# Optimization experiments

Hardware: AMD Instinct MI355X
Metric: run time of the kernel (lower is better)

Reference implementation:

```python
import jax, jax.numpy as jnp
import numpy as np
from jax import lax

B, C, H, W = 8, 256, 32, 32
HEADS = 8
NUM_OFF = 9
OFF_SCALE = 0.1


def setup_inputs() -> dict:
    key = jax.random.key(0)
    ks = jax.random.split(key, 8)
    f = lambda k, s, sc: jax.random.normal(k, s, dtype=jnp.float32) * sc
    return {
        'query_map': f(ks[0], (B, C, H, W), 1.0),
        'kv_map': f(ks[1], (B, C, H, W), 1.0),
        'Wq': f(ks[2], (C, C), C ** -0.5),
        'Wk': f(ks[3], (C, C), C ** -0.5),
        'Wv': f(ks[4], (C, C), C ** -0.5),
        'Woff1': f(ks[5], (C // 2, C, 3, 3), (C * 9) ** -0.5),
        'boff1': jnp.zeros((C // 2,), jnp.float32),
        'Woff2': f(ks[6], (NUM_OFF * 2, C // 2), (C // 2) ** -0.5),
        'boff2': jnp.zeros((NUM_OFF * 2,), jnp.float32),
        'Wout': f(ks[7], (C, C), C ** -0.5),
        'bout': jnp.zeros((C,), jnp.float32),
    }


def grid_sample_bilinear_border(img, grid):
    """img: (B,C,H,W); grid: (B,H,W,2) with (x,y) in [-1,1], align_corners=True,
    padding_mode='border'. Returns (B,C,H,W)."""
    Bn, Cn, Hn, Wn = img.shape
    x = (grid[..., 0] + 1.0) * 0.5 * (Wn - 1)
    y = (grid[..., 1] + 1.0) * 0.5 * (Hn - 1)
    # border padding: clamp continuous coords into the valid range
    x = jnp.clip(x, 0.0, Wn - 1)
    y = jnp.clip(y, 0.0, Hn - 1)
    x0 = jnp.floor(x)
    y0 = jnp.floor(y)
    wx = x - x0
    wy = y - y0
    x0i = x0.astype(jnp.int32)
    y0i = y0.astype(jnp.int32)
    x1i = jnp.minimum(x0i + 1, Wn - 1)
    y1i = jnp.minimum(y0i + 1, Hn - 1)
    flat = img.reshape(Bn, Cn, Hn * Wn)

    def gat(iy, ix):
        idx = (iy * Wn + ix).reshape(Bn, 1, -1)  # broadcasts over channels
        return jnp.take_along_axis(flat, idx, axis=2)

    v00 = gat(y0i, x0i)
    v01 = gat(y0i, x1i)
    v10 = gat(y1i, x0i)
    v11 = gat(y1i, x1i)
    wxf = wx.reshape(Bn, 1, -1)
    wyf = wy.reshape(Bn, 1, -1)
    out = (v00 * (1 - wxf) + v01 * wxf) * (1 - wyf) + (v10 * (1 - wxf) + v11 * wxf) * wyf
    return out.reshape(Bn, Cn, Hn, Wn)


def reference(query_map, kv_map, Wq, Wk, Wv, Woff1, boff1, Woff2, boff2, Wout, bout):
    Bn, Cn, Hn, Wn = query_map.shape
    hd = Cn // HEADS
    # 1x1 conv projections as channel einsums
    q = jnp.einsum('oc,bchw->bohw', Wq, query_map)
    # offset network: 3x3 conv -> relu -> 1x1 conv
    h1 = lax.conv_general_dilated(q, Woff1, (1, 1), 'SAME',
                                  dimension_numbers=('NCHW', 'OIHW', 'NCHW'))
    h1 = jax.nn.relu(h1 + boff1[None, :, None, None])
    offsets = jnp.einsum('oc,bchw->bohw', Woff2, h1) + boff2[None, :, None, None]
    offsets = offsets.reshape(Bn, NUM_OFF, 2, Hn, Wn)
    offset = offsets[:, 0] * OFF_SCALE  # (B,2,H,W); ch0 -> x, ch1 -> y
    # normalized base grid in [-1,1] (align_corners=True convention)
    gx = jnp.linspace(-1.0, 1.0, Wn, dtype=q.dtype)[None, :]  # (1,W)
    gy = jnp.linspace(-1.0, 1.0, Hn, dtype=q.dtype)[:, None]  # (H,1)
    vx = gx[None] + offset[:, 0]  # (B,H,W)
    vy = gy[None] + offset[:, 1]
    vgrid = jnp.stack([vx, vy], axis=-1)  # (B,H,W,2)
    kv_sampled = grid_sample_bilinear_border(kv_map, vgrid)
    k = jnp.einsum('oc,bchw->bohw', Wk, kv_sampled)
    v = jnp.einsum('oc,bchw->bohw', Wv, kv_sampled)
    # (B,C,H,W) -> (B,heads,HW,hd)
    def to_heads(t):
        return t.reshape(Bn, HEADS, hd, Hn * Wn).transpose(0, 1, 3, 2)
    qh, kh, vh = to_heads(q), to_heads(k), to_heads(v)
    scale = hd ** -0.5
    attn = jnp.einsum('bhqd,bhkd->bhqk', qh, kh) * scale
    attn = jax.nn.softmax(attn, axis=-1)
    out = jnp.einsum('bhqk,bhkd->bhqd', attn, vh)
    out = out.transpose(0, 1, 3, 2).reshape(Bn, Cn, Hn, Wn)
    out = jnp.einsum('oc,bchw->bohw', Wout, out) + bout[None, :, None, None]
    return out
```

## Files before the change

### kernel.cpp

```cpp
#include <hip/hip_runtime.h>

#define HW_ 1024

typedef __attribute__((ext_vector_type(8))) short bf16x8;
typedef __attribute__((ext_vector_type(4))) short bf16x4;
typedef __attribute__((ext_vector_type(4))) float f32x4;

__device__ inline unsigned short f2bf(float f) {
  unsigned int u = __float_as_uint(f);
  u += 0x7FFF + ((u >> 16) & 1);
  return (unsigned short)(u >> 16);
}
__device__ inline unsigned short f2bf_fast(float f) {
  return (unsigned short)((__float_as_uint(f) + 0x8000u) >> 16);
}
__device__ inline float bf2f(unsigned short h) {
  return __uint_as_float(((unsigned int)h) << 16);
}
__device__ inline void async_copy16(const void* g, void* l) {
  __builtin_amdgcn_global_load_lds(
      (const __attribute__((address_space(1))) unsigned int*)g,
      (__attribute__((address_space(3))) unsigned int*)l, 16, 0, 0);
}

__global__ __launch_bounds__(256) void fused0(
    const float* __restrict__ kv,
    const float* __restrict__ Wq, const float* __restrict__ Wk,
    const float* __restrict__ Wv, const float* __restrict__ Wo,
    const float* __restrict__ Woff1, const float* __restrict__ Xf,
    short* __restrict__ WH, short* __restrict__ WL, short* __restrict__ wb,
    float* __restrict__ kvT,
    short* __restrict__ Yt, short* __restrict__ Yh2, short* __restrict__ Yl2)
{
  __shared__ float T[256][33];
  __shared__ short Bsh[32][40];
  __shared__ short Bsl[32][40];
  const int bid = blockIdx.x, t = threadIdx.x;

  if (bid < 512) {
    const int w    = t >> 6;
    const int lane = t & 63;
    const int ln   = lane & 15;
    const int qd   = lane >> 4;
    const int bp0  = (bid & 255) * 32;
    const int om   = (bid >> 8) * 128 + w * 32;
    const int bB   = bp0 >> 10, p0l = bp0 & 1023;

    f32x4 acc[2][2] = {};
#pragma unroll
    for (int k0 = 0; k0 < 256; k0 += 32) {
      __syncthreads();
      {
        int pp = t & 31, cg = t >> 5;
        float fv[4];
#pragma unroll
        for (int j = 0; j < 4; ++j)
          fv[j] = Xf[((size_t)(bB * 256 + k0 + cg * 4 + j)) * HW_ + p0l + pp];
        bf16x4 h4, l4;
#pragma unroll
        for (int j = 0; j < 4; ++j) {
          unsigned short h = f2bf(fv[j]);
          h4[j] = (short)h;
          l4[j] = (short)f2bf(fv[j] - bf2f(h));
        }
        *(bf16x4*)&Bsh[pp][cg * 4] = h4;
        *(bf16x4*)&Bsl[pp][cg * 4] = l4;
      }
      __syncthreads();

      bf16x8 Ah[2], Al[2], Bh[2], Bl[2];
#pragma unroll
      for (int mt = 0; mt < 2; ++mt) {
        const float* ws = &Wq[((size_t)(om + mt * 16 + ln)) * 256 + k0 + qd * 8];
        float4 fa = *(const float4*)ws;
        float4 fb = *(const float4*)(ws + 4);
        float f8[8] = {fa.x, fa.y, fa.z, fa.w, fb.x, fb.y, fb.z, fb.w};
#pragma unroll
        for (int j = 0; j < 8; ++j) {
          unsigned short h = f2bf(f8[j]);
          Ah[mt][j] = (short)h;
          Al[mt][j] = (short)f2bf(f8[j] - bf2f(h));
        }
      }
#pragma unroll
      for (int nt = 0; nt < 2; ++nt) {
        Bh[nt] = *(const bf16x8*)&Bsh[nt * 16 + ln][qd * 8];
        Bl[nt] = *(const bf16x8*)&Bsl[nt * 16 + ln][qd * 8];
      }
#pragma unroll
      for (int mt = 0; mt < 2; ++mt)
#pragma unroll
        for (int nt = 0; nt < 2; ++nt) {
          acc[mt][nt] = __builtin_amdgcn_mfma_f32_16x16x32_bf16(Ah[mt], Bh[nt], acc[mt][nt], 0, 0, 0);
          acc[mt][nt] = __builtin_amdgcn_mfma_f32_16x16x32_bf16(Ah[mt], Bl[nt], acc[mt][nt], 0, 0, 0);
          acc[mt][nt] = __builtin_amdgcn_mfma_f32_16x16x32_bf16(Al[mt], Bh[nt], acc[mt][nt], 0, 0, 0);
        }
    }

    const float sc = 0.25506063286f;
#pragma unroll
    for (int mt = 0; mt < 2; ++mt)
#pragma unroll
      for (int nt = 0; nt < 2; ++nt) {
        int bp = bp0 + nt * 16 + ln;
        int b = bp >> 10, p = bp & 1023;
#pragma unroll
        for (int i = 0; i < 4; ++i) {
          int o = om + mt * 16 + qd * 4 + i;
          int h = o >> 5, d = o & 31;
          Yt[(((size_t)(b * 8 + h)) * 1024 + p) * 32 + d] = (short)f2bf(acc[mt][nt][i] * sc);
        }
        int ob = om + mt * 16 + qd * 4;
        bf16x4 h4, l4;
#pragma unroll
        for (int i = 0; i < 4; ++i) {
          float f = acc[mt][nt][i];
          unsigned short h = f2bf(f);
          h4[i] = (short)h;
          l4[i] = (short)f2bf(f - bf2f(h));
        }
        *(bf16x4*)&Yh2[(size_t)bp * 256 + ob] = h4;
        *(bf16x4*)&Yl2[(size_t)bp * 256 + ob] = l4;
      }

  } else if (bid < 768) {
    int tb = bid - 512;
    int b = tb >> 5, p0 = (tb & 31) * 32;
    int pp = t & 31, cg = t >> 5;
#pragma unroll
    for (int i = 0; i < 32; ++i) {
      int c = cg * 32 + i;
      T[c][pp] = kv[((size_t)(b * 256 + c)) * HW_ + p0 + pp];
    }
    __syncthreads();
#pragma unroll
    for (int r = 0; r < 8; ++r) {
      int e = t + 256 * r;
      int c4 = (e & 63) * 4, pp2 = e >> 6;
      float4 v4;
      v4.x = T[c4 + 0][pp2];
      v4.y = T[c4 + 1][pp2];
      v4.z = T[c4 + 2][pp2];
      v4.w = T[c4 + 3][pp2];
      *(float4*)&kvT[((size_t)(b * 1024 + p0 + pp2)) * 256 + c4] = v4;
    }
  } else if (bid < 960) {
    int b2 = bid - 768;
    int mat = b2 >> 6;
    int loc = (b2 & 63) * 1024 + t * 4;
    const float* W = (mat == 0) ? Wk : (mat == 1) ? Wv : Wo;
    float4 f4 = *(const float4*)&W[loc];
    float f[4] = {f4.x, f4.y, f4.z, f4.w};
    bf16x4 h4, l4;
#pragma unroll
    for (int j = 0; j < 4; ++j) {
      unsigned short h = f2bf(f[j]);
      h4[j] = (short)h;
      l4[j] = (short)f2bf(f[j] - bf2f(h));
    }
    *(bf16x4*)&WH[(mat + 1) * 65536 + loc] = h4;
    *(bf16x4*)&WL[(mat + 1) * 65536 + loc] = l4;
  } else {
    int e0 = (bid - 960) * 1024 + t * 4;
#pragma unroll
    for (int j = 0; j < 4; ++j) {
      int e = e0 + j;
      int c = e & 255;
      int o = (e >> 8) & 127;
      int tap = e >> 15;
      wb[e] = (short)f2bf(Woff1[((size_t)(o * 256 + c)) * 9 + tap]);
    }
  }
}

__global__ __launch_bounds__(512) void convkv(
    const short* __restrict__ wb, const float* __restrict__ bias,
    const float* __restrict__ W2, const float* __restrict__ b2,
    const short* __restrict__ xh, const short* __restrict__ xl,
    const float* __restrict__ kvT,
    const short* __restrict__ WH, const short* __restrict__ WL,
    short* __restrict__ kt, short* __restrict__ vt)
{
  __shared__ short Xs[2][3][34][40];
  __shared__ float red[8][32][2];
  __shared__ short XsH[32][264];
  __shared__ short XsL[32][264];
  __shared__ float2 crd[32];
  const int id   = blockIdx.x;
  const int b    = id & 7;
  const int y0   = id >> 3;
  const int t    = threadIdx.x;
  const int w    = t >> 6;
  const int lane = t & 63;
  const int ln   = lane & 15;
  const int qd   = lane >> 4;
  const int o0   = w * 16;
  const int bp0  = (b * 32 + y0) * 32;

  f32x4 acc[2] = {};
  for (int c0 = 0; c0 < 256; c0 += 32) {
    __syncthreads();
#pragma unroll
    for (int i = 0; i < 2; ++i) {
      int e = t + 512 * i;
      if (e < 768) {
        int oct = e & 3;
        int x   = (e >> 2) & 31;
        int r   = (e >> 7) % 3;
        int hl  = e / 384;
        int yy  = y0 + r - 1;
        bf16x8 val = {};
        if (yy >= 0 && yy < 32) {
          const short* src = hl ? xl : xh;
          val = *(const bf16x8*)&src[((size_t)((b * 32 + yy) * 32 + x)) * 256 + c0 + oct * 8];
        }
        *(bf16x8*)&Xs[hl][r][x + 1][oct * 8] = val;
      }
    }
    if (t < 48) {
      int oct = t & 3;
      int col = ((t >> 2) & 1) ? 33 : 0;
      int r   = (t >> 3) % 3;
      int hl  = t / 24;
      bf16x8 zz = {};
      *(bf16x8*)&Xs[hl][r][col][oct * 8] = zz;
    }
    __syncthreads();

#pragma unroll
    for (int tap = 0; tap < 9; ++tap) {
      const int ky = tap / 3, kx = tap % 3;
      bf16x8 afr = *(const bf16x8*)&wb[((size_t)(tap * 128 + o0 + ln)) * 256
                                       + c0 + qd * 8];
#pragma unroll
      for (int nt = 0; nt < 2; ++nt) {
        int hc = nt * 16 + ln + kx;
        bf16x8 bh = *(const bf16x8*)&Xs[0][ky][hc][qd * 8];
        bf16x8 bl = *(const bf16x8*)&Xs[1][ky][hc][qd * 8];
        acc[nt] = __builtin_amdgcn_mfma_f32_16x16x32_bf16(afr, bh, acc[nt], 0, 0, 0);
        acc[nt] = __builtin_amdgcn_mfma_f32_16x16x32_bf16(afr, bl, acc[nt], 0, 0, 0);
      }
    }
  }

  {
    float ps0[2] = {0.f, 0.f}, ps1[2] = {0.f, 0.f};
#pragma unroll
    for (int i = 0; i < 4; ++i) {
      int o = o0 + qd * 4 + i;
      float bo = bias[o];
      float w2a = W2[o], w2b = W2[128 + o];
#pragma unroll
      for (int nt = 0; nt < 2; ++nt) {
        float h = fmaxf(acc[nt][i] + bo, 0.f);
        ps0[nt] += w2a * h;
        ps1[nt] += w2b * h;
      }
    }
#pragma unroll
    for (int msk = 16; msk < 64; msk <<= 1) {
      ps0[0] += __shfl_xor(ps0[0], msk, 64);
      ps0[1] += __shfl_xor(ps0[1], msk, 64);
      ps1[0] += __shfl_xor(ps1[0], msk, 64);
      ps1[1] += __shfl_xor(ps1[1], msk, 64);
    }
    if (qd == 0) {
#pragma unroll
      for (int nt = 0; nt < 2; ++nt) {
        red[w][nt * 16 + ln][0] = ps0[nt];
        red[w][nt * 16 + ln][1] = ps1[nt];
      }
    }
  }
  __syncthreads();
  if (t < 32) {
    float a0 = red[0][t][0] + red[1][t][0] + red[2][t][0] + red[3][t][0];
    float a1 = red[4][t][0] + red[5][t][0] + red[6][t][0] + red[7][t][0];
    float c0s = (a0 + a1) + b2[0];
    float d0 = red[0][t][1] + red[1][t][1] + red[2][t][1] + red[3][t][1];
    float d1 = red[4][t][1] + red[5][t][1] + red[6][t][1] + red[7][t][1];
    float c1s = (d0 + d1) + b2[1];
    float gx = -1.f + 2.f * (float)t / 31.f;
    float gy = -1.f + 2.f * (float)y0 / 31.f;
    float vx = gx + 0.1f * c0s;
    float vy = gy + 0.1f * c1s;
    float px = fminf(fmaxf((vx + 1.f) * 0.5f * 31.f, 0.f), 31.f);
    float py = fminf(fmaxf((vy + 1.f) * 0.5f * 31.f, 0.f), 31.f);
    crd[t] = make_float2(px, py);
  }
  __syncthreads();

#pragma unroll
  for (int it = 0; it < 2; ++it) {
    int e = t + 512 * it;
    int oct = e & 31, row = e >> 5;
    float2 cd = crd[row];
    float x0f = floorf(cd.x), y0f = floorf(cd.y);
    float wx = cd.x - x0f, wy = cd.y - y0f;
    int x0 = (int)x0f, y0i = (int)y0f;
    int x1 = min(x0 + 1, 31), y1 = min(y0i + 1, 31);
    float w00 = (1.f - wx) * (1.f - wy), w01 = wx * (1.f - wy);
    float w10 = (1.f - wx) * wy,         w11 = wx * wy;
    const float* r00 = &kvT[((size_t)(b * 1024 + y0i * 32 + x0)) * 256 + oct * 8];
    const float* r01 = &kvT[((size_t)(b * 1024 + y0i * 32 + x1)) * 256 + oct * 8];
    const float* r10 = &kvT[((size_t)(b * 1024 + y1 * 32 + x0)) * 256 + oct * 8];
    const float* r11 = &kvT[((size_t)(b * 1024 + y1 * 32 + x1)) * 256 + oct * 8];
    float4 a00 = *(const float4*)r00, b00 = *(const float4*)(r00 + 4);
    float4 a01 = *(const float4*)r01, b01 = *(const float4*)(r01 + 4);
    float4 a10 = *(const float4*)r10, b10 = *(const float4*)(r10 + 4);
    float4 a11 = *(const float4*)r11, b11 = *(const float4*)(r11 + 4);
    float v[8];
    v[0] = a00.x * w00 + a01.x * w01 + a10.x * w10 + a11.x * w11;
    v[1] = a00.y * w00 + a01.y * w01 + a10.y * w10 + a11.y * w11;
    v[2] = a00.z * w00 + a01.z * w01 + a10.z * w10 + a11.z * w11;
    v[3] = a00.w * w00 + a01.w * w01 + a10.w * w10 + a11.w * w11;
    v[4] = b00.x * w00 + b01.x * w01 + b10.x * w10 + b11.x * w11;
    v[5] = b00.y * w00 + b01.y * w01 + b10.y * w10 + b11.y * w11;
    v[6] = b00.z * w00 + b01.z * w01 + b10.z * w10 + b11.z * w11;
    v[7] = b00.w * w00 + b01.w * w01 + b10.w * w10 + b11.w * w11;
    bf16x8 h8, l8;
#pragma unroll
    for (int j = 0; j < 8; ++j) {
      unsigned short h = f2bf(v[j]);
      h8[j] = (short)h;
      l8[j] = (short)f2bf(v[j] - bf2f(h));
    }
    *(bf16x8*)&XsH[row][oct * 8] = h8;
    *(bf16x8*)&XsL[row][oct * 8] = l8;
  }
  __syncthreads();

  const int mat  = w >> 2;
  const short* WAh = WH + (mat ? 131072 : 65536);
  const short* WAl = WL + (mat ? 131072 : 65536);
  const int om = (w & 3) * 64;

  f32x4 acg[4][2] = {};
#pragma unroll
  for (int k0 = 0; k0 < 256; k0 += 32) {
    bf16x8 Bh[2], Bl[2];
#pragma unroll
    for (int nt = 0; nt < 2; ++nt) {
      Bh[nt] = *(const bf16x8*)&XsH[nt * 16 + ln][k0 + qd * 8];
      Bl[nt] = *(const bf16x8*)&XsL[nt * 16 + ln][k0 + qd * 8];
    }
#pragma unroll
    for (int mt = 0; mt < 4; ++mt) {
      size_t wi = ((size_t)(om + mt * 16 + ln)) * 256 + k0 + qd * 8;
      bf16x8 Ah = *(const bf16x8*)&WAh[wi];
      bf16x8 Al = *(const bf16x8*)&WAl[wi];
#pragma unroll
      for (int nt = 0; nt < 2; ++nt) {
        acg[mt][nt] = __builtin_amdgcn_mfma_f32_16x16x32_bf16(Ah, Bh[nt], acg[mt][nt], 0, 0, 0);
        acg[mt][nt] = __builtin_amdgcn_mfma_f32_16x16x32_bf16(Ah, Bl[nt], acg[mt][nt], 0, 0, 0);
        acg[mt][nt] = __builtin_amdgcn_mfma_f32_16x16x32_bf16(Al, Bh[nt], acg[mt][nt], 0, 0, 0);
      }
    }
  }

#pragma unroll
  for (int mt = 0; mt < 4; ++mt)
#pragma unroll
    for (int nt = 0; nt < 2; ++nt) {
      int p  = bp0 + nt * 16 + ln;
      int pl = p & 1023;
      int jt = pl >> 6, jl = pl & 63;
#pragma unroll
      for (int i = 0; i < 4; ++i) {
        int oc = om + mt * 16 + qd * 4 + i;
        unsigned short val = f2bf(acg[mt][nt][i]);
        int bhead = b * 8 + (oc >> 5), d = oc & 31;
        if (mat == 0) {
          int cd2 = (d >> 3) ^ ((jl >> 2) & 3);
          kt[((((size_t)(bhead * 16 + jt)) * 64 + jl) * 4 + cd2) * 8 + (d & 7)] = (short)val;
        } else {
          int jjs = ((jl & 15) << 2) | (jl >> 4);
          int cj = (jjs >> 3) ^ (d & 7);
          vt[((((size_t)(bhead * 16 + jt)) * 32 + d) * 8 + cj) * 8 + (jjs & 7)] = (short)val;
        }
      }
    }
}

__global__ __launch_bounds__(256) void attn_mfma(
    const short* __restrict__ qt, const short* __restrict__ kt,
    const short* __restrict__ vt, short* __restrict__ aoh,
    short* __restrict__ aol)
{
  __shared__ __align__(16) short Ks[2][2048];
  __shared__ __align__(16) short Vs[2][2048];
  __shared__ __align__(16) short P[4][32][72];
  const int t    = threadIdx.x;
  const int w    = t >> 6;
  const int lane = t & 63;
  const int ln   = lane & 15;
  const int qd   = lane >> 4;
  const int id   = blockIdx.x;
  const int b    = id & 7;
  const int rem  = id >> 3;
  const int h    = rem & 7;
  const int qc   = rem >> 3;
  const int bh   = b * 8 + h;
  const int qbase = qc * 128 + w * 16;

  const short* ktb = kt + (size_t)bh * 32768;
  const short* vtb = vt + (size_t)bh * 32768;

  bf16x8 aq[2];
  aq[0] = *(const bf16x8*)&qt[((size_t)(bh * 1024 + qbase + ln)) * 32 + qd * 8];
  aq[1] = *(const bf16x8*)&qt[((size_t)(bh * 1024 + qbase + 64 + ln)) * 32 + qd * 8];

  f32x4 acc[2][2] = {};
  float lacc[2][4] = {};
  const f32x4 zero = {0.f, 0.f, 0.f, 0.f};

  const int stoff = w * 512 + lane * 8;
  const int ldoff = w * 512;

  async_copy16(&ktb[stoff], &Ks[0][ldoff]);
  async_copy16(&vtb[stoff], &Vs[0][ldoff]);
  __syncthreads();

  for (int jt = 0; jt < 16; ++jt) {
    const int cur = jt & 1, nxt = cur ^ 1;
    if (jt < 15) {
      async_copy16(&ktb[(jt + 1) * 2048 + stoff], &Ks[nxt][ldoff]);
      async_copy16(&vtb[(jt + 1) * 2048 + stoff], &Vs[nxt][ldoff]);
    }

    bf16x8 bk[4], bv[2][2];
#pragma unroll
    for (int kk = 0; kk < 4; ++kk)
      bk[kk] = *(const bf16x8*)&Ks[cur][((kk * 16 + ln) * 4 + (qd ^ ((ln >> 2) & 3))) * 8];
#pragma unroll
    for (int kc = 0; kc < 2; ++kc)
#pragma unroll
      for (int ds = 0; ds < 2; ++ds)
        bv[kc][ds] = *(const bf16x8*)&Vs[cur][((ds * 16 + ln) * 8 + ((kc * 4 + qd) ^ (ln & 7))) * 8];

#pragma unroll
    for (int qf = 0; qf < 2; ++qf) {
      f32x4 s[4];
      __builtin_amdgcn_s_setprio(1);
#pragma unroll
      for (int kk = 0; kk < 4; ++kk)
        s[kk] = __builtin_amdgcn_mfma_f32_16x16x32_bf16(aq[qf], bk[kk], zero, 0, 0, 0);
      __builtin_amdgcn_s_setprio(0);

#pragma unroll
      for (int i = 0; i < 4; ++i) {
        float p0 = __builtin_amdgcn_exp2f(s[0][i]);
        float p1 = __builtin_amdgcn_exp2f(s[1][i]);
        float p2 = __builtin_amdgcn_exp2f(s[2][i]);
        float p3 = __builtin_amdgcn_exp2f(s[3][i]);
        s[0][i] = p0; s[1][i] = p1; s[2][i] = p2; s[3][i] = p3;
        lacc[qf][i] += (p0 + p1) + (p2 + p3);
      }
#pragma unroll
      for (int i = 0; i < 4; ++i) {
        bf16x4 p4;
#pragma unroll
        for (int kk = 0; kk < 4; ++kk) p4[kk] = (short)f2bf_fast(s[kk][i]);
        *(bf16x4*)&P[w][qf * 16 + qd * 4 + i][4 * ln] = p4;
      }
      __builtin_amdgcn_s_setprio(1);
#pragma unroll
      for (int kc = 0; kc < 2; ++kc) {
        bf16x8 ap = *(const bf16x8*)&P[w][qf * 16 + ln][kc * 32 + qd * 8];
#pragma unroll
        for (int ds = 0; ds < 2; ++ds)
          acc[qf][ds] = __builtin_amdgcn_mfma_f32_16x16x32_bf16(ap, bv[kc][ds], acc[qf][ds], 0, 0, 0);
      }
      __builtin_amdgcn_s_setprio(0);
    }

    __syncthreads();
  }

  const int bb = bh >> 3, hh2 = bh & 7;
#pragma unroll
  for (int qf = 0; qf < 2; ++qf)
#pragma unroll
    for (int i = 0; i < 4; ++i) {
      float l = lacc[qf][i];
      l += __shfl_xor(l, 1, 64);
      l += __shfl_xor(l, 2, 64);
      l += __shfl_xor(l, 4, 64);
      l += __shfl_xor(l, 8, 64);
      float inv = 1.f / l;
      int qrow = qbase + qf * 64 + qd * 4 + i;
#pragma unroll
      for (int ds = 0; ds < 2; ++ds) {
        float v = acc[qf][ds][i] * inv;
        unsigned short hv = f2bf(v);
        size_t idx = ((size_t)(bb * 1024 + qrow)) * 256 + hh2 * 32 + ds * 16 + ln;
        aoh[idx] = (short)hv;
        aol[idx] = (short)f2bf(v - bf2f(hv));
      }
    }
}

__global__ __launch_bounds__(256) void gemm_out(
    const short* __restrict__ Wh, const short* __restrict__ Wl,
    const short* __restrict__ Xh, const short* __restrict__ Xl,
    const float* __restrict__ bias, float* __restrict__ Yf)
{
  const int t    = threadIdx.x;
  const int w    = t >> 6;
  const int lane = t & 63;
  const int ln   = lane & 15;
  const int qd   = lane >> 4;
  const int bp0  = blockIdx.x * 32;
  const int om   = blockIdx.y * 128 + w * 32;

  f32x4 acc[2][2] = {};
#pragma unroll
  for (int k0 = 0; k0 < 256; k0 += 32) {
    bf16x8 Ah[2], Al[2], Bh[2], Bl[2];
#pragma unroll
    for (int mt = 0; mt < 2; ++mt) {
      size_t wi = ((size_t)(om + mt * 16 + ln)) * 256 + k0 + qd * 8;
      Ah[mt] = *(const bf16x8*)&Wh[wi];
      Al[mt] = *(const bf16x8*)&Wl[wi];
    }
#pragma unroll
    for (int nt = 0; nt < 2; ++nt) {
      size_t xi = ((size_t)(bp0 + nt * 16 + ln)) * 256 + k0 + qd * 8;
      Bh[nt] = *(const bf16x8*)&Xh[xi];
      Bl[nt] = *(const bf16x8*)&Xl[xi];
    }
#pragma unroll
    for (int mt = 0; mt < 2; ++mt)
#pragma unroll
      for (int nt = 0; nt < 2; ++nt) {
        acc[mt][nt] = __builtin_amdgcn_mfma_f32_16x16x32_bf16(Ah[mt], Bh[nt], acc[mt][nt], 0, 0, 0);
        acc[mt][nt] = __builtin_amdgcn_mfma_f32_16x16x32_bf16(Ah[mt], Bl[nt], acc[mt][nt], 0, 0, 0);
        acc[mt][nt] = __builtin_amdgcn_mfma_f32_16x16x32_bf16(Al[mt], Bh[nt], acc[mt][nt], 0, 0, 0);
      }
  }

#pragma unroll
  for (int mt = 0; mt < 2; ++mt)
#pragma unroll
    for (int i = 0; i < 4; ++i) {
      int o = om + mt * 16 + qd * 4 + i;
      float bo = bias[o];
#pragma unroll
      for (int nt = 0; nt < 2; ++nt) {
        int bp = bp0 + nt * 16 + ln;
        int b = bp >> 10, p = bp & 1023;
        Yf[((size_t)(b * 256 + o)) * HW_ + p] = acc[mt][nt][i] + bo;
      }
    }
}

extern "C" void kernel_launch(void* const* d_in, const int* in_sizes, int n_in,
                              void* d_out, int out_size, void* d_ws, size_t ws_size,
                              hipStream_t stream)
{
  const float* query_map = (const float*)d_in[0];
  const float* kv_map    = (const float*)d_in[1];
  const float* Wq        = (const float*)d_in[2];
  const float* Wk        = (const float*)d_in[3];
  const float* Wv        = (const float*)d_in[4];
  const float* Woff1     = (const float*)d_in[5];
  const float* boff1     = (const float*)d_in[6];
  const float* Woff2     = (const float*)d_in[7];
  const float* boff2     = (const float*)d_in[8];
  const float* Wout      = (const float*)d_in[9];
  const float* bout      = (const float*)d_in[10];
  float* out = (float*)d_out;
  char* base = (char*)d_ws;

  const size_t MB = 1u << 20;
  short* qt     = (short*)(base + 1 * MB);
  short* kt     = (short*)(base + 5 * MB);
  short* vt     = (short*)(base + 9 * MB);
  short* bufBh  = (short*)(base + 13 * MB);
  short* bufBl  = (short*)(base + 17 * MB);
  short* wb     = (short*)(base + 21 * MB);
  short* WH     = (short*)(base + 22 * MB);
  short* WL     = (short*)(base + 23 * MB);
  float* kvT    = (float*)(base + 24 * MB);

  fused0<<<dim3(1248), dim3(256), 0, stream>>>(kv_map, Wq, Wk, Wv, Wout, Woff1,
                                               query_map, WH, WL, wb, kvT,
                                               qt, bufBh, bufBl);
  convkv<<<dim3(256), dim3(512), 0, stream>>>(wb, boff1, Woff2, boff2,
                                              bufBh, bufBl, kvT, WH, WL, kt, vt);
  attn_mfma<<<dim3(512), dim3(256), 0, stream>>>(qt, kt, vt, bufBh, bufBl);
  gemm_out<<<dim3(256, 2), dim3(256), 0, stream>>>(WH + 196608, WL + 196608,
                                                   bufBh, bufBl, bout, out);
}
```

Measured before the change: 183.3 us.

## Stage full-channel conv halo once and split-K offset conv across warps

The 3x3 offset convolution in convkv now loads all 256 channels of the three input rows (hi and lo bf16 parts) into LDS in one pass, replacing the eight-iteration channel loop that synced twice per iteration. Each warp now computes a 32x32 output tile over half of the channels, reusing each B fragment across two A fragments. The two channel halves are summed through a shared-memory partial buffer that reuses the XsH region. This cuts barriers and LDS traffic per MFMA, but raises LDS use substantially, which may lower occupancy.

```diff
diff --git a/kernel.cpp b/kernel.cpp
--- a/kernel.cpp
+++ b/kernel.cpp
@@ -181,10 +181,10 @@
     const short* __restrict__ WH, const short* __restrict__ WL,
     short* __restrict__ kt, short* __restrict__ vt)
 {
-  __shared__ short Xs[2][3][34][40];
-  __shared__ float red[8][32][2];
+  __shared__ short Xs[2][3][34][264];
   __shared__ short XsH[32][264];
   __shared__ short XsL[32][264];
+  __shared__ float red[4][32][2];
   __shared__ float2 crd[32];
   const int id   = blockIdx.x;
   const int b    = id & 7;
@@ -194,69 +194,107 @@
   const int lane = t & 63;
   const int ln   = lane & 15;
   const int qd   = lane >> 4;
-  const int o0   = w * 16;
   const int bp0  = (b * 32 + y0) * 32;
 
-  f32x4 acc[2] = {};
-  for (int c0 = 0; c0 < 256; c0 += 32) {
-    __syncthreads();
-#pragma unroll
-    for (int i = 0; i < 2; ++i) {
+  {
+    bf16x8 v[12];
+#pragma unroll
+    for (int i = 0; i < 12; ++i) {
       int e = t + 512 * i;
-      if (e < 768) {
-        int oct = e & 3;
-        int x   = (e >> 2) & 31;
-        int r   = (e >> 7) % 3;
-        int hl  = e / 384;
-        int yy  = y0 + r - 1;
-        bf16x8 val = {};
-        if (yy >= 0 && yy < 32) {
-          const short* src = hl ? xl : xh;
-          val = *(const bf16x8*)&src[((size_t)((b * 32 + yy) * 32 + x)) * 256 + c0 + oct * 8];
-        }
-        *(bf16x8*)&Xs[hl][r][x + 1][oct * 8] = val;
-      }
-    }
-    if (t < 48) {
-      int oct = t & 3;
-      int col = ((t >> 2) & 1) ? 33 : 0;
-      int r   = (t >> 3) % 3;
-      int hl  = t / 24;
+      int oct = e & 31;
+      int x   = (e >> 5) & 31;
+      int rr  = e >> 10;
+      int hl  = rr / 3, r = rr % 3;
+      int yy  = y0 + r - 1;
+      bf16x8 val = {};
+      if (yy >= 0 && yy < 32) {
+        const short* src = hl ? xl : xh;
+        val = *(const bf16x8*)&src[((size_t)((b * 32 + yy) * 32 + x)) * 256 + oct * 8];
+      }
+      v[i] = val;
+    }
+#pragma unroll
+    for (int i = 0; i < 12; ++i) {
+      int e = t + 512 * i;
+      int oct = e & 31;
+      int x   = (e >> 5) & 31;
+      int rr  = e >> 10;
+      int hl  = rr / 3, r = rr % 3;
+      *(bf16x8*)&Xs[hl][r][x + 1][oct * 8] = v[i];
+    }
+    if (t < 384) {
+      int oct  = t & 31;
+      int colw = (t >> 5) & 1;
+      int rr   = t >> 6;
+      int hl   = rr / 3, r = rr % 3;
       bf16x8 zz = {};
-      *(bf16x8*)&Xs[hl][r][col][oct * 8] = zz;
-    }
-    __syncthreads();
-
+      *(bf16x8*)&Xs[hl][r][colw ? 33 : 0][oct * 8] = zz;
+    }
+  }
+  __syncthreads();
+
+  const int chh = w >> 2;
+  const int ow  = w & 3;
+  const int o0c = ow * 32;
+  f32x4 acc[2][2] = {};
+#pragma unroll
+  for (int c0s = 0; c0s < 4; ++c0s) {
+    const int c0 = chh * 128 + c0s * 32;
 #pragma unroll
     for (int tap = 0; tap < 9; ++tap) {
       const int ky = tap / 3, kx = tap % 3;
-      bf16x8 afr = *(const bf16x8*)&wb[((size_t)(tap * 128 + o0 + ln)) * 256
-                                       + c0 + qd * 8];
+      bf16x8 afr[2];
+#pragma unroll
+      for (int m = 0; m < 2; ++m)
+        afr[m] = *(const bf16x8*)&wb[((size_t)(tap * 128 + o0c + m * 16 + ln)) * 256
+                                     + c0 + qd * 8];
 #pragma unroll
       for (int nt = 0; nt < 2; ++nt) {
         int hc = nt * 16 + ln + kx;
-        bf16x8 bh = *(const bf16x8*)&Xs[0][ky][hc][qd * 8];
-        bf16x8 bl = *(const bf16x8*)&Xs[1][ky][hc][qd * 8];
-        acc[nt] = __builtin_amdgcn_mfma_f32_16x16x32_bf16(afr, bh, acc[nt], 0, 0, 0);
-        acc[nt] = __builtin_amdgcn_mfma_f32_16x16x32_bf16(afr, bl, acc[nt], 0, 0, 0);
-      }
-    }
-  }
-
-  {
+        bf16x8 bh = *(const bf16x8*)&Xs[0][ky][hc][c0 + qd * 8];
+        bf16x8 bl = *(const bf16x8*)&Xs[1][ky][hc][c0 + qd * 8];
+#pragma unroll
+        for (int m = 0; m < 2; ++m) {
+          acc[m][nt] = __builtin_amdgcn_mfma_f32_16x16x32_bf16(afr[m], bh, acc[m][nt], 0, 0, 0);
+          acc[m][nt] = __builtin_amdgcn_mfma_f32_16x16x32_bf16(afr[m], bl, acc[m][nt], 0, 0, 0);
+        }
+      }
+    }
+  }
+
+  float* ps = (float*)&XsH[0][0];
+  if (w >= 4) {
+#pragma unroll
+    for (int m = 0; m < 2; ++m)
+#pragma unroll
+      for (int nt = 0; nt < 2; ++nt)
+        *(f32x4*)&ps[(((w - 4) * 64 + lane) * 4 + m * 2 + nt) * 4] = acc[m][nt];
+  }
+  __syncthreads();
+
+  if (w < 4) {
     float ps0[2] = {0.f, 0.f}, ps1[2] = {0.f, 0.f};
 #pragma unroll
-    for (int i = 0; i < 4; ++i) {
-      int o = o0 + qd * 4 + i;
-      float bo = bias[o];
-      float w2a = W2[o], w2b = W2[128 + o];
-#pragma unroll
-      for (int nt = 0; nt < 2; ++nt) {
-        float h = fmaxf(acc[nt][i] + bo, 0.f);
-        ps0[nt] += w2a * h;
-        ps1[nt] += w2b * h;
-      }
-    }
+    for (int m = 0; m < 2; ++m)
+#pragma unroll
+      for (int nt = 0; nt < 2; ++nt) {
+        f32x4 p = *(const f32x4*)&ps[((w * 64 + lane) * 4 + m * 2 + nt) * 4];
+        acc[m][nt] += p;
+      }
+#pragma unroll
+    for (int m = 0; m < 2; ++m)
+#pragma unroll
+      for (int i = 0; i < 4; ++i) {
+        int o = o0c + m * 16 + qd * 4 + i;
+        float bo = bias[o];
+        float w2a = W2[o], w2b = W2[128 + o];
+#pragma unroll
+        for (int nt = 0; nt < 2; ++nt) {
+          float h = fmaxf(acc[m][nt][i] + bo, 0.f);
+          ps0[nt] += w2a * h;
+          ps1[nt] += w2b * h;
+        }
+      }
 #pragma unroll
     for (int msk = 16; msk < 64; msk <<= 1) {
       ps0[0] += __shfl_xor(ps0[0], msk, 64);
@@ -274,12 +312,8 @@
   }
   __syncthreads();
   if (t < 32) {
-    float a0 = red[0][t][0] + red[1][t][0] + red[2][t][0] + red[3][t][0];
-    float a1 = red[4][t][0] + red[5][t][0] + red[6][t][0] + red[7][t][0];
-    float c0s = (a0 + a1) + b2[0];
-    float d0 = red[0][t][1] + red[1][t][1] + red[2][t][1] + red[3][t][1];
-    float d1 = red[4][t][1] + red[5][t][1] + red[6][t][1] + red[7][t][1];
-    float c1s = (d0 + d1) + b2[1];
+    float c0s = (red[0][t][0] + red[1][t][0]) + (red[2][t][0] + red[3][t][0]) + b2[0];
+    float c1s = (red[0][t][1] + red[1][t][1]) + (red[2][t][1] + red[3][t][1]) + b2[1];
     float gx = -1.f + 2.f * (float)t / 31.f;
     float gy = -1.f + 2.f * (float)y0 / 31.f;
     float vx = gx + 0.1f * c0s;
```

Result: faster. 179.5 us (-2.1%).
